# Optimization experiments

Hardware: AMD Instinct MI355X
Metric: run time of the kernel (lower is better)

## Reference

```python
import jax, jax.numpy as jnp
import numpy as np

B = 128          # batch
D = 2048         # original_dim
P = 16000        # projection_dim


def _count_sketch_matrix(key, d, p):
    """Dense count-sketch matrix: one +/-1 per row at a random column.
    Mirrors the torch init: col ~ randint(0, p-1), sign = 2*randint(0,2)-1."""
    k_idx, k_sgn = jax.random.split(key)
    idx = jax.random.randint(k_idx, (d,), 0, p - 1)            # torch uses high=p-1 (exclusive)
    sgn = (2 * jax.random.randint(k_sgn, (d,), 0, 2) - 1).astype(jnp.float32)
    C = jnp.zeros((d, p), dtype=jnp.float32)
    return C.at[jnp.arange(d), idx].set(sgn)


def setup_inputs() -> dict:
    key = jax.random.key(0)
    kx1, kx2, kc1, kc2 = jax.random.split(key, 4)
    x1 = jax.random.normal(kx1, (B, D), dtype=jnp.float32)
    x2 = jax.random.normal(kx2, (B, D), dtype=jnp.float32)
    C1 = _count_sketch_matrix(kc1, D, P)
    C2 = _count_sketch_matrix(kc2, D, P)
    return {"x1": x1, "x2": x2, "C1": C1, "C2": C2}


def reference(x1, x2, C1, C2):
    # Count-sketch projections (dense mm, as in the original module)
    y1 = x1 @ C1                      # [B, P]
    y2 = x2 @ C2                      # [B, P]
    # Circular convolution via FFT -> elementwise complex multiply -> IFFT.
    # Original takes only the real part of the IFFT output.
    f1 = jnp.fft.fft(y1, axis=-1)
    f2 = jnp.fft.fft(y2, axis=-1)
    phi = jnp.fft.ifft(f1 * f2, axis=-1).real.astype(jnp.float32)
    return phi                        # [B, P]
```

## Files before the change

### kernel.cpp

```cpp
#include <hip/hip_runtime.h>

#define NFFT 16000
#define BATCH 128
#define DIM 2048

__device__ __forceinline__ float2 cmul(float2 a, float2 b) {
    return make_float2(a.x * b.x - a.y * b.y, a.x * b.y + a.y * b.x);
}
__device__ __forceinline__ float2 cadd(float2 a, float2 b) { return make_float2(a.x + b.x, a.y + b.y); }
__device__ __forceinline__ float2 csub(float2 a, float2 b) { return make_float2(a.x - b.x, a.y - b.y); }
__device__ __forceinline__ float2 cis(float ang) { return make_float2(__cosf(ang), __sinf(ang)); }

__device__ __forceinline__ int rev5_3(int n) {
    int d0 = n % 5, r = n / 5;
    int d1 = r % 5, d2 = r / 5;
    return d0 * 25 + d1 * 5 + d2;
}
__device__ __forceinline__ int rev7(int x) { return (int)(__brev((unsigned)x) >> 25); }

__device__ __forceinline__ float2 shfl2(float2 v, int lane) {
    return make_float2(__shfl(v.x, lane), __shfl(v.y, lane));
}
__device__ __forceinline__ float2 shfl2_xor(float2 v, int mask) {
    return make_float2(__shfl_xor(v.x, mask), __shfl_xor(v.y, mask));
}

__device__ __forceinline__ float2 conjG(float2 Zk, float2 Zm) {
    float u = (Zk.x * Zk.x - Zk.y * Zk.y) - (Zm.x * Zm.x - Zm.y * Zm.y);
    float v = 2.f * (Zk.x * Zk.y + Zm.x * Zm.y);
    return make_float2(0.25f * v, 0.25f * u);
}

__device__ __forceinline__ void dif128(float2& x0, float2& x1, const float2* tw, int l) {
    {
        float2 a = x0, b = x1;
        x0 = cadd(a, b);
        x1 = cmul(csub(a, b), tw[0]);
    }
    int s = 1;
    #pragma unroll
    for (int m = 32; m >= 1; m >>= 1, ++s) {
        float2 w = tw[s];
        float2 o0 = shfl2_xor(x0, m), o1 = shfl2_xor(x1, m);
        if (l & m) {
            x0 = cmul(csub(o0, x0), w);
            x1 = cmul(csub(o1, x1), w);
        } else {
            x0 = cadd(x0, o0);
            x1 = cadd(x1, o1);
        }
    }
}

__global__ void extract_sketch(const float* __restrict__ C1, const float* __restrict__ C2,
                               int* __restrict__ idx1, float* __restrict__ sgn1,
                               int* __restrict__ idx2, float* __restrict__ sgn2) {
    int gwave = (blockIdx.x * blockDim.x + threadIdx.x) >> 6;
    int lane = threadIdx.x & 63;
    if (gwave >= 2 * DIM) return;
    const float* row;
    int* idxp; float* sgnp; int d;
    if (gwave < DIM) { d = gwave;       row = C1 + (size_t)d * NFFT; idxp = idx1; sgnp = sgn1; }
    else             { d = gwave - DIM; row = C2 + (size_t)d * NFFT; idxp = idx2; sgnp = sgn2; }
    for (int step = 0; step < 16; ++step) {
        int off0 = step * 1024 + lane * 4;
        float4 v[4];
        #pragma unroll
        for (int c = 0; c < 4; ++c) {
            int off = off0 + c * 256;
            v[c] = (off < NFFT) ? *reinterpret_cast<const float4*>(row + off)
                                : make_float4(0.f, 0.f, 0.f, 0.f);
        }
        bool found = false;
        #pragma unroll
        for (int c = 0; c < 4; ++c) {
            float4 w = v[c];
            if (w.x != 0.f || w.y != 0.f || w.z != 0.f || w.w != 0.f) {
                int off = off0 + c * 256;
                int j; float s;
                if (w.x != 0.f)      { j = 0; s = w.x; }
                else if (w.y != 0.f) { j = 1; s = w.y; }
                else if (w.z != 0.f) { j = 2; s = w.z; }
                else                 { j = 3; s = w.w; }
                idxp[d] = off + j;
                sgnp[d] = s;
                found = true;
            }
        }
        if (__any(found)) return;
    }
}

__global__ void __launch_bounds__(1024) fused_fft(
        const float* __restrict__ x1, const float* __restrict__ x2,
        const int* __restrict__ idx1, const float* __restrict__ sgn1,
        const int* __restrict__ idx2, const float* __restrict__ sgn2,
        float* __restrict__ out) {
    __shared__ float2 A[16000];
    const int b = blockIdx.x;
    const int tid = threadIdx.x;

    for (int i = tid; i < 16000; i += 1024) A[i] = make_float2(0.f, 0.f);
    __syncthreads();

    const float* x1b = x1 + (size_t)b * DIM;
    const float* x2b = x2 + (size_t)b * DIM;
    for (int d = tid; d < DIM; d += 1024) {
        int p1 = idx1[d];
        atomicAdd(&A[(p1 & 127) * 125 + rev5_3(p1 >> 7)].x, sgn1[d] * x1b[d]);
        int p2 = idx2[d];
        atomicAdd(&A[(p2 & 127) * 125 + rev5_3(p2 >> 7)].y, sgn2[d] * x2b[d]);
    }
    __syncthreads();

    const float C1_5 = 0.30901699437494742f, S1_5 = 0.95105651629515357f;
    const float C2_5 = -0.80901699437494745f, S2_5 = 0.58778525229247312f;
    const float2 w5tab[5] = { make_float2(1.f, 0.f),
                              make_float2(C1_5, -S1_5), make_float2(C2_5, -S2_5),
                              make_float2(C2_5,  S2_5), make_float2(C1_5,  S1_5) };

    #pragma unroll
    for (int s = 0; s < 3; ++s) {
        const int m = (s == 0) ? 1 : (s == 1) ? 5 : 25;
        const float angstep = -6.28318530717958647692f / (float)(5 * m);
        for (int task = tid; task < 128 * 25; task += 1024) {
            int row = task / 25;
            int bf = task - row * 25;
            int t = bf % m, blk = bf / m;
            int base = row * 125 + blk * (5 * m) + t;
            float2 xv[5];
            #pragma unroll
            for (int r = 0; r < 5; ++r) xv[r] = A[base + r * m];
            if (m > 1) {
                float2 w1 = cis(angstep * (float)t);
                float2 w2 = cmul(w1, w1), w3 = cmul(w2, w1), w4 = cmul(w2, w2);
                xv[1] = cmul(xv[1], w1); xv[2] = cmul(xv[2], w2);
                xv[3] = cmul(xv[3], w3); xv[4] = cmul(xv[4], w4);
            }
            float2 y[5];
            #pragma unroll
            for (int qq = 0; qq < 5; ++qq) {
                float2 acc = xv[0];
                #pragma unroll
                for (int r = 1; r < 5; ++r) {
                    float2 t2 = cmul(xv[r], w5tab[(qq * r) % 5]);
                    acc.x += t2.x; acc.y += t2.y;
                }
                y[qq] = acc;
            }
            #pragma unroll
            for (int qq = 0; qq < 5; ++qq) A[base + qq * m] = y[qq];
        }
        __syncthreads();
    }

    const int w = tid >> 6, l = tid & 63;
    const float PI_F = 3.14159265358979323846f;
    const float ANGN = -6.28318530717958647692f / 16000.0f;

    float2 tw[7];
    tw[0] = cis(-PI_F / 64.0f * (float)l);
    {
        int m = 32;
        #pragma unroll
        for (int s = 1; s < 7; ++s, m >>= 1)
            tw[s] = cis(-PI_F / (float)m * (float)(l & (m - 1)));
    }

    for (int tsk = w; tsk < 63; tsk += 16) {
        const int c = tsk, cm = tsk ? 125 - tsk : 0;

        float2 a0 = cmul(A[l * 125 + c],        cis(ANGN * (float)(l * c)));
        float2 a1 = cmul(A[(l + 64) * 125 + c], cis(ANGN * (float)((l + 64) * c)));
        dif128(a0, a1, tw, l);
        float2 b0, b1;
        if (tsk) {
            b0 = cmul(A[l * 125 + cm],        cis(ANGN * (float)(l * cm)));
            b1 = cmul(A[(l + 64) * 125 + cm], cis(ANGN * (float)((l + 64) * cm)));
            dif128(b0, b1, tw, l);
        }

        const int e  = rev7(l);
        const int lp = rev7(126 - e);

        float2 gA0, gA1, gB0, gB1;
        if (tsk) {
            float2 zm0 = shfl2(b1, lp);
            float2 zm1 = shfl2(b0, lp);
            gA0 = conjG(a0, zm0);
            gA1 = conjG(a1, zm1);
            float2 ym0 = shfl2(a1, lp);
            float2 ym1 = shfl2(a0, lp);
            gB0 = conjG(b0, ym0);
            gB1 = conjG(b1, ym1);
        } else {
            int hz = rev7((128 - e) & 127);
            float2 zm0 = shfl2(a0, hz);
            float2 zm1 = shfl2(a1, lp);
            gA0 = conjG(a0, zm0);
            gA1 = conjG(a1, zm1);
            gB0 = gB1 = make_float2(0.f, 0.f);
        }

        const int q = rev7(l & 62);
        {
            float2 t00 = shfl2(gA0, q),     t10 = shfl2(gA1, q);
            float2 t01 = shfl2(gA0, q + 1), t11 = shfl2(gA1, q + 1);
            float2 p0 = (l & 1) ? t10 : t00;
            float2 p1 = (l & 1) ? t11 : t01;
            dif128(p0, p1, tw, l);
            p0 = cmul(p0, cis(ANGN * (float)(c * e)));
            p1 = cmul(p1, cis(ANGN * (float)(c * (e + 1))));
            A[e * 125 + c] = p0;
            A[(e + 1) * 125 + c] = p1;
        }
        if (tsk) {
            float2 t00 = shfl2(gB0, q),     t10 = shfl2(gB1, q);
            float2 t01 = shfl2(gB0, q + 1), t11 = shfl2(gB1, q + 1);
            float2 p0 = (l & 1) ? t10 : t00;
            float2 p1 = (l & 1) ? t11 : t01;
            dif128(p0, p1, tw, l);
            p0 = cmul(p0, cis(ANGN * (float)(cm * e)));
            p1 = cmul(p1, cis(ANGN * (float)(cm * (e + 1))));
            A[e * 125 + cm] = p0;
            A[(e + 1) * 125 + cm] = p1;
        }
    }
    __syncthreads();

    #pragma unroll
    for (int s = 0; s < 3; ++s) {
        const int L = (s == 0) ? 125 : (s == 1) ? 25 : 5;
        const int m = L / 5;
        const float angstep = -6.28318530717958647692f / (float)L;
        for (int task = tid; task < 128 * 25; task += 1024) {
            int row = task / 25;
            int bf = task - row * 25;
            int t = bf % m, blk = bf / m;
            int base = row * 125 + blk * L + t;
            float2 xv[5];
            #pragma unroll
            for (int r = 0; r < 5; ++r) xv[r] = A[base + r * m];
            float2 y[5];
            #pragma unroll
            for (int qq = 0; qq < 5; ++qq) {
                float2 acc = xv[0];
                #pragma unroll
                for (int r = 1; r < 5; ++r) {
                    float2 t2 = cmul(xv[r], w5tab[(qq * r) % 5]);
                    acc.x += t2.x; acc.y += t2.y;
                }
                y[qq] = acc;
            }
            if (L > 5) {
                float2 w1 = cis(angstep * (float)t);
                float2 w2 = cmul(w1, w1), w3 = cmul(w2, w1), w4 = cmul(w2, w2);
                y[1] = cmul(y[1], w1); y[2] = cmul(y[2], w2);
                y[3] = cmul(y[3], w3); y[4] = cmul(y[4], w4);
            }
            #pragma unroll
            for (int qq = 0; qq < 5; ++qq) A[base + qq * m] = y[qq];
        }
        __syncthreads();
    }

    const float invN = 1.0f / (float)NFFT;
    float* outb = out + (size_t)b * NFFT;
    for (int i = tid; i < 16000; i += 1024) {
        int j1 = i & 127, s = i >> 7;
        outb[j1 + 128 * rev5_3(s)] = A[j1 * 125 + s].x * invN;
    }
}

extern "C" void kernel_launch(void* const* d_in, const int* in_sizes, int n_in,
                              void* d_out, int out_size, void* d_ws, size_t ws_size,
                              hipStream_t stream) {
    (void)in_sizes; (void)n_in; (void)out_size; (void)ws_size;
    const float* x1 = (const float*)d_in[0];
    const float* x2 = (const float*)d_in[1];
    const float* C1 = (const float*)d_in[2];
    const float* C2 = (const float*)d_in[3];
    float* out = (float*)d_out;

    char* w = (char*)d_ws;
    int*    idx1 = (int*)  (w);
    float*  sgn1 = (float*)(w + 8192);
    int*    idx2 = (int*)  (w + 16384);
    float*  sgn2 = (float*)(w + 24576);

    extract_sketch<<<(2 * DIM) / 4, 256, 0, stream>>>(C1, C2, idx1, sgn1, idx2, sgn2);
    fused_fft     <<<BATCH, 1024, 0, stream>>>(x1, x2, idx1, sgn1, idx2, sgn2, out);
}
```

Measured before the change: 311.5 us.

## Split fused FFT kernel into column-FFT and row-FFT kernels via workspace

The single per-batch fused FFT kernel becomes two kernels. The first launches two blocks per batch row, each scattering and running radix-5 column FFTs on half the rows, applying twiddles and writing to a global workspace. The second loads that intermediate into LDS and does the remaining radix-128 and inverse stages. This doubles block-level parallelism for the first phase (128 blocks on a large GPU) at the cost of an extra global round-trip of 128x16000 complex values and an additional launch.

```diff
diff --git a/kernel.cpp b/kernel.cpp
--- a/kernel.cpp
+++ b/kernel.cpp
@@ -91,25 +91,25 @@
     }
 }
 
-__global__ void __launch_bounds__(1024) fused_fft(
+__global__ void __launch_bounds__(1024) k1_colfft(
         const float* __restrict__ x1, const float* __restrict__ x2,
         const int* __restrict__ idx1, const float* __restrict__ sgn1,
         const int* __restrict__ idx2, const float* __restrict__ sgn2,
-        float* __restrict__ out) {
-    __shared__ float2 A[16000];
-    const int b = blockIdx.x;
+        float2* __restrict__ U) {
+    __shared__ float2 S[64 * 125];
+    const int b = blockIdx.x >> 1, h = blockIdx.x & 1;
     const int tid = threadIdx.x;
 
-    for (int i = tid; i < 16000; i += 1024) A[i] = make_float2(0.f, 0.f);
+    for (int i = tid; i < 64 * 125; i += 1024) S[i] = make_float2(0.f, 0.f);
     __syncthreads();
 
     const float* x1b = x1 + (size_t)b * DIM;
     const float* x2b = x2 + (size_t)b * DIM;
     for (int d = tid; d < DIM; d += 1024) {
-        int p1 = idx1[d];
-        atomicAdd(&A[(p1 & 127) * 125 + rev5_3(p1 >> 7)].x, sgn1[d] * x1b[d]);
-        int p2 = idx2[d];
-        atomicAdd(&A[(p2 & 127) * 125 + rev5_3(p2 >> 7)].y, sgn2[d] * x2b[d]);
+        int p1 = idx1[d]; int n1a = p1 & 127;
+        if ((n1a >> 6) == h) atomicAdd(&S[(n1a & 63) * 125 + rev5_3(p1 >> 7)].x, sgn1[d] * x1b[d]);
+        int p2 = idx2[d]; int n1b = p2 & 127;
+        if ((n1b >> 6) == h) atomicAdd(&S[(n1b & 63) * 125 + rev5_3(p2 >> 7)].y, sgn2[d] * x2b[d]);
     }
     __syncthreads();
 
@@ -118,19 +118,18 @@
     const float2 w5tab[5] = { make_float2(1.f, 0.f),
                               make_float2(C1_5, -S1_5), make_float2(C2_5, -S2_5),
                               make_float2(C2_5,  S2_5), make_float2(C1_5,  S1_5) };
-
     #pragma unroll
     for (int s = 0; s < 3; ++s) {
         const int m = (s == 0) ? 1 : (s == 1) ? 5 : 25;
         const float angstep = -6.28318530717958647692f / (float)(5 * m);
-        for (int task = tid; task < 128 * 25; task += 1024) {
+        for (int task = tid; task < 64 * 25; task += 1024) {
             int row = task / 25;
             int bf = task - row * 25;
             int t = bf % m, blk = bf / m;
             int base = row * 125 + blk * (5 * m) + t;
             float2 xv[5];
             #pragma unroll
-            for (int r = 0; r < 5; ++r) xv[r] = A[base + r * m];
+            for (int r = 0; r < 5; ++r) xv[r] = S[base + r * m];
             if (m > 1) {
                 float2 w1 = cis(angstep * (float)t);
                 float2 w2 = cmul(w1, w1), w3 = cmul(w2, w1), w4 = cmul(w2, w2);
@@ -149,10 +148,32 @@
                 y[qq] = acc;
             }
             #pragma unroll
-            for (int qq = 0; qq < 5; ++qq) A[base + qq * m] = y[qq];
+            for (int qq = 0; qq < 5; ++qq) S[base + qq * m] = y[qq];
         }
         __syncthreads();
     }
+
+    const float ANGN = -6.28318530717958647692f / 16000.0f;
+    float2* Ub = U + (size_t)b * NFFT;
+    for (int i = tid; i < 64 * 125; i += 1024) {
+        int n1l = i / 125, k2 = i - n1l * 125;
+        int n1 = h * 64 + n1l;
+        Ub[n1 * 125 + k2] = cmul(S[i], cis(ANGN * (float)(n1 * k2)));
+    }
+}
+
+__global__ void __launch_bounds__(1024) k2_fused(const float2* __restrict__ U,
+                                                 float* __restrict__ out) {
+    __shared__ __align__(16) float2 A[16000];
+    const int b = blockIdx.x;
+    const int tid = threadIdx.x;
+
+    {
+        const float4* src = reinterpret_cast<const float4*>(U + (size_t)b * NFFT);
+        float4* dst = reinterpret_cast<float4*>(A);
+        for (int i = tid; i < 8000; i += 1024) dst[i] = src[i];
+    }
+    __syncthreads();
 
     const int w = tid >> 6, l = tid & 63;
     const float PI_F = 3.14159265358979323846f;
@@ -170,13 +191,13 @@
     for (int tsk = w; tsk < 63; tsk += 16) {
         const int c = tsk, cm = tsk ? 125 - tsk : 0;
 
-        float2 a0 = cmul(A[l * 125 + c],        cis(ANGN * (float)(l * c)));
-        float2 a1 = cmul(A[(l + 64) * 125 + c], cis(ANGN * (float)((l + 64) * c)));
+        float2 a0 = A[l * 125 + c];
+        float2 a1 = A[(l + 64) * 125 + c];
         dif128(a0, a1, tw, l);
         float2 b0, b1;
         if (tsk) {
-            b0 = cmul(A[l * 125 + cm],        cis(ANGN * (float)(l * cm)));
-            b1 = cmul(A[(l + 64) * 125 + cm], cis(ANGN * (float)((l + 64) * cm)));
+            b0 = A[l * 125 + cm];
+            b1 = A[(l + 64) * 125 + cm];
             dif128(b0, b1, tw, l);
         }
 
@@ -228,6 +249,12 @@
     }
     __syncthreads();
 
+    const float C1_5 = 0.30901699437494742f, S1_5 = 0.95105651629515357f;
+    const float C2_5 = -0.80901699437494745f, S2_5 = 0.58778525229247312f;
+    const float2 w5tab[5] = { make_float2(1.f, 0.f),
+                              make_float2(C1_5, -S1_5), make_float2(C2_5, -S2_5),
+                              make_float2(C2_5,  S2_5), make_float2(C1_5,  S1_5) };
+
     #pragma unroll
     for (int s = 0; s < 3; ++s) {
         const int L = (s == 0) ? 125 : (s == 1) ? 25 : 5;
@@ -287,7 +314,9 @@
     float*  sgn1 = (float*)(w + 8192);
     int*    idx2 = (int*)  (w + 16384);
     float*  sgn2 = (float*)(w + 24576);
+    float2* U    = (float2*)(w + 32768);
 
     extract_sketch<<<(2 * DIM) / 4, 256, 0, stream>>>(C1, C2, idx1, sgn1, idx2, sgn2);
-    fused_fft     <<<BATCH, 1024, 0, stream>>>(x1, x2, idx1, sgn1, idx2, sgn2, out);
-}
+    k1_colfft     <<<BATCH * 2, 1024, 0, stream>>>(x1, x2, idx1, sgn1, idx2, sgn2, U);
+    k2_fused      <<<BATCH, 1024, 0, stream>>>(U, out);
+}
```

Result: no change. 310.7 us (-0.3%).
